# Kernel tuning notes

Hardware: AMD Instinct MI355X
Metric: run time of the kernel (lower is better)

The kernel has to match this reference:

```python
import jax, jax.numpy as jnp
import numpy as np

B, C, T = 128, 295, 2048
D1 = 270
NUM_SUBJECTS = 64

def setup_inputs() -> dict:
    key = jax.random.key(0)
    k_x, k_s, k_w1, k_b1, k_ws = jax.random.split(key, 5)
    X = jax.random.normal(k_x, (B, C, T), dtype=jnp.float32)
    subject_idxs = jax.random.randint(k_s, (B,), 0, NUM_SUBJECTS)
    W1 = jax.random.normal(k_w1, (D1, C), dtype=jnp.float32) * 0.05
    b1 = jax.random.normal(k_b1, (D1,), dtype=jnp.float32) * 0.05
    Ws = jax.random.normal(k_ws, (NUM_SUBJECTS, D1, D1), dtype=jnp.float32) * 0.05
    return {"X": X, "subject_idxs": subject_idxs, "W1": W1, "b1": b1, "Ws": Ws}

def reference(X, subject_idxs, W1, b1, Ws):
    # Shared 1x1 conv: pointwise channel mix C -> D1 with bias.  [B, D1, T]
    y = jnp.einsum('dc,bct->bdt', W1, X) + b1[None, :, None]
    # Top-1 expert dispatch: gather each sample's subject matrix. [B, D1, D1]
    W_sel = Ws[subject_idxs]
    # Per-sample 1x1 conv (batched GEMM), no bias.            [B, D1, T]
    out = jnp.einsum('bed,bdt->bet', W_sel, y)
    return out
```

## Files before the change

kernel.cpp:

```cpp
#include <hip/hip_runtime.h>
#include <hip/hip_bf16.h>

#define NSUBJ 64
#define CIN   295
#define DD    270
#define TT    2048
#define BB    128

#define WF_PER_S  92160
#define WF_PER_KS 9216
#define W1T_PER_KS 10240

typedef __attribute__((ext_vector_type(8))) short bf16x8;
typedef __attribute__((ext_vector_type(4))) float f32x4;
typedef unsigned short u16;

__device__ __forceinline__ u16 f2bf(float f) {
    return __bfloat16_as_ushort(__float2bfloat16(f));
}

__device__ __forceinline__ void glds16(const void* g, void* lds_base) {
    __builtin_amdgcn_global_load_lds(
        (const __attribute__((address_space(1))) unsigned int*)g,
        (__attribute__((address_space(3))) unsigned int*)lds_base, 16, 0, 0);
}

#define WAITV(N) asm volatile("s_waitcnt vmcnt(" #N ")" ::: "memory")
#define BAR()    __builtin_amdgcn_s_barrier()
#define SB()     __builtin_amdgcn_sched_barrier(0)

__global__ __launch_bounds__(256) void k_prep_w1(const float* __restrict__ W1,
                                                 const float* __restrict__ b1,
                                                 u16* __restrict__ W1t)
{
    const int idx = blockIdx.x * 256 + threadIdx.x;
    const int ks = idx / W1T_PER_KS;
    const int r  = idx - ks * W1T_PER_KS;
    const int kq = r / 2560;
    const int c  = (r - kq * 2560) >> 3;
    const int k8 = r & 7;
    const int d  = ks * 32 + kq * 8 + k8;
    float v = 0.f;
    if (d < DD) {
        if (c < CIN) v = W1[d * CIN + c];
        else if (c == CIN) v = b1[d];
    }
    W1t[idx] = f2bf(v);
}

__global__ __launch_bounds__(256, 1) void k_fuse_w(const float* __restrict__ Ws,
                                                   const u16* __restrict__ W1t,
                                                   u16* __restrict__ Wf)
{
    __shared__ u16 Aw[3072];
    __shared__ u16 Bw[10240];
    const int tid = threadIdx.x, lane = tid & 63, wid = tid >> 6;
    const int wm = wid >> 1, wn = wid & 1;
    const int mt = blockIdx.x, s = blockIdx.y;
    const int e0 = mt * 96;
    const float* Wsb = Ws + (size_t)s * DD * DD;

    f32x4 acc[3][10];
#pragma unroll
    for (int i = 0; i < 3; ++i)
#pragma unroll
        for (int j = 0; j < 10; ++j) acc[i][j] = (f32x4){0.f, 0.f, 0.f, 0.f};

    for (int ks = 0; ks < 9; ++ks) {
        const int k0 = ks * 32;
#pragma unroll
        for (int ci = 0; ci < 3; ++ci) {
            const int id = tid + ci * 256;
            const int m = id >> 3, q = id & 7;
            const int e = e0 + m, d = k0 + q * 4;
            float2 v01 = {0.f, 0.f}, v23 = {0.f, 0.f};
            if (e < DD) {
                if (d < DD)     v01 = *(const float2*)(Wsb + (size_t)e * DD + d);
                if (d + 2 < DD) v23 = *(const float2*)(Wsb + (size_t)e * DD + d + 2);
            }
            ushort4 h;
            h.x = f2bf(v01.x); h.y = f2bf(v01.y); h.z = f2bf(v23.x); h.w = f2bf(v23.y);
            *(ushort4*)(&Aw[(q >> 1) * 768 + m * 8 + (q & 1) * 4]) = h;
        }
#pragma unroll
        for (int k5 = 0; k5 < 5; ++k5) {
            const int seg = wid * 5 + k5;
            glds16(W1t + (size_t)ks * W1T_PER_KS + seg * 512 + lane * 8, &Bw[seg * 512]);
        }
        __syncthreads();
        bf16x8 af[3];
#pragma unroll
        for (int i = 0; i < 3; ++i)
            af[i] = *(const bf16x8*)(&Aw[(lane >> 4) * 768 + (wm * 48 + i * 16 + (lane & 15)) * 8]);
#pragma unroll
        for (int j = 0; j < 10; ++j) {
            const bf16x8 bfj = *(const bf16x8*)(&Bw[(lane >> 4) * 2560 + (wn * 160 + j * 16 + (lane & 15)) * 8]);
#pragma unroll
            for (int i = 0; i < 3; ++i)
                acc[i][j] = __builtin_amdgcn_mfma_f32_16x16x32_bf16(af[i], bfj, acc[i][j], 0, 0, 0);
        }
        __syncthreads();
    }
    const int rb = (lane >> 4) * 4, cc = lane & 15;
#pragma unroll
    for (int i = 0; i < 3; ++i) {
#pragma unroll
        for (int r = 0; r < 4; ++r) {
            const int e = e0 + wm * 48 + i * 16 + rb + r;
#pragma unroll
            for (int j = 0; j < 10; ++j) {
                const int c = wn * 160 + j * 16 + cc;
                Wf[(size_t)s * WF_PER_S + (c >> 5) * WF_PER_KS + ((c >> 3) & 3) * 2304
                   + e * 8 + (c & 7)] = f2bf(acc[i][j][r]);
            }
        }
    }
}

__global__ __launch_bounds__(256, 2) void k_main(const float* __restrict__ X,
                                                 const int* __restrict__ subj,
                                                 const u16* __restrict__ Wf,
                                                 float* __restrict__ out)
{
    __shared__ u16   Am[3][9216];
    __shared__ float Xm[3][2048];
    const int tid = threadIdx.x, lane = tid & 63, wid = tid >> 6;
    const int wm = wid >> 1, wn = wid & 1;
    const int hw = blockIdx.x;
    const int w  = (hw & 7) * 512 + (hw >> 3);
    const int b  = w >> 5, nt = w & 31;
    const int t0 = nt * 64;
    const int s = subj[b];
    const float* Xb = X + (size_t)b * CIN * TT;
    const u16* WfA = Wf + (size_t)s * WF_PER_S;
    const int g = lane >> 4;

    f32x4 acc[9][2];
#pragma unroll
    for (int i = 0; i < 9; ++i)
#pragma unroll
        for (int j = 0; j < 2; ++j) acc[i][j] = (f32x4){0.f, 0.f, 0.f, 0.f};

#define STAGEA(KS, BUF)                                                     \
    {                                                                       \
        _Pragma("unroll")                                                   \
        for (int k5 = 0; k5 < 5; ++k5) {                                    \
            const int seg = wid + 4 * k5;                                   \
            if (seg < 18)                                                   \
                glds16(WfA + (size_t)(KS) * WF_PER_KS + seg * 512 + lane * 8,\
                       &Am[BUF][seg * 512]);                                \
        }                                                                   \
    }
#define STAGEX(KS, BUF)                                                     \
    {                                                                       \
        _Pragma("unroll")                                                   \
        for (int k2 = 0; k2 < 2; ++k2) {                                    \
            const int seg = wid * 2 + k2;                                   \
            const int cr0 = (KS) * 32 + seg * 4 + g;                        \
            const int cr  = (cr0 < CIN) ? cr0 : (CIN - 1);                  \
            const int sc  = (lane & 15) ^ (((seg >> 1) & 3) << 2);          \
            glds16(Xb + (size_t)cr * TT + t0 + sc * 4,                      \
                   &Xm[BUF][seg * 256]);                                    \
        }                                                                   \
    }
#define WAITSTEP()  { if (wid < 2) WAITV(7); else WAITV(6); }

#define COMPUTE(BUF, LAST)                                                  \
    {                                                                       \
        const float* Xc = &Xm[BUF][0];                                      \
        bf16x8 bfr[2];                                                      \
        _Pragma("unroll")                                                   \
        for (int j = 0; j < 2; ++j) {                                       \
            const int tsw = (wn * 32 + j * 16 + (lane & 15)) ^ (g << 4);    \
            bf16x8 bb;                                                      \
            _Pragma("unroll")                                               \
            for (int q = 0; q < 8; ++q) {                                   \
                float v = Xc[(g * 8 + q) * 64 + tsw];                       \
                if (LAST) {                                                 \
                    if (q == 7)      v = (g == 0) ? 1.0f : 0.0f;            \
                    else if (g > 0)  v = 0.0f;                              \
                }                                                           \
                bb[q] = (short)f2bf(v);                                     \
            }                                                               \
            bfr[j] = bb;                                                    \
        }                                                                   \
        _Pragma("unroll")                                                   \
        for (int i = 0; i < 9; ++i) {                                       \
            const bf16x8 af = *(const bf16x8*)(&Am[BUF][g * 2304 + (wm * 144 + i * 16 + (lane & 15)) * 8]); \
            acc[i][0] = __builtin_amdgcn_mfma_f32_16x16x32_bf16(af, bfr[0], acc[i][0], 0, 0, 0); \
            acc[i][1] = __builtin_amdgcn_mfma_f32_16x16x32_bf16(af, bfr[1], acc[i][1], 0, 0, 0); \
        }                                                                   \
    }

    STAGEA(0, 0); STAGEX(0, 0); SB();
    STAGEA(1, 1); STAGEX(1, 1); SB();
    WAITSTEP();
    BAR();

#define STEP(K)                                                             \
    {                                                                       \
        STAGEA((K) + 2, ((K) + 2) % 3); STAGEX((K) + 2, ((K) + 2) % 3); SB();\
        COMPUTE((K) % 3, 0);                                                \
        WAITSTEP();                                                         \
        BAR();                                                              \
    }
    STEP(0) STEP(1) STEP(2) STEP(3) STEP(4) STEP(5) STEP(6) STEP(7)
    COMPUTE(2, 0);
    WAITV(0);
    BAR();
    COMPUTE(0, 1);

    const int rb = g * 4, cc = lane & 15;
#pragma unroll
    for (int i = 0; i < 9; ++i) {
#pragma unroll
        for (int r = 0; r < 4; ++r) {
            const int e = wm * 144 + i * 16 + rb + r;
            if (e < DD) {
#pragma unroll
                for (int j = 0; j < 2; ++j) {
                    const int t = t0 + wn * 32 + j * 16 + cc;
                    out[((size_t)b * DD + e) * TT + t] = acc[i][j][r];
                }
            }
        }
    }
#undef STAGEA
#undef STAGEX
#undef WAITSTEP
#undef COMPUTE
#undef STEP
}

extern "C" void kernel_launch(void* const* d_in, const int* in_sizes, int n_in,
                              void* d_out, int out_size, void* d_ws, size_t ws_size,
                              hipStream_t stream) {
    const float* X    = (const float*)d_in[0];
    const int*   subj = (const int*)d_in[1];
    const float* W1   = (const float*)d_in[2];
    const float* b1   = (const float*)d_in[3];
    const float* Ws   = (const float*)d_in[4];
    float* out = (float*)d_out;

    u16* Wf  = (u16*)d_ws;
    u16* W1t = (u16*)((char*)d_ws + (size_t)NSUBJ * WF_PER_S * 2);

    k_prep_w1<<<dim3(360), 256, 0, stream>>>(W1, b1, W1t);
    k_fuse_w<<<dim3(3, NSUBJ), 256, 0, stream>>>(Ws, W1t, Wf);
    k_main<<<dim3(TT / 64 * BB), 256, 0, stream>>>(X, subj, Wf, out);
}
```

Measured before the change: 184.8 us.

## Make main kernel persistent over eight tiles with cross-tile prefetch

The main GEMM kernel now launches 512 blocks, and each block loops over eight consecutive output tiles instead of handling one tile per block. The first two K-stages of the next tile are prefetched while the last stages and epilogue of the current tile run, and the triple-buffer pointers are rotated between tiles. This targets block launch, prologue and pipeline drain costs. The trade-offs are fewer resident blocks relative to CU count, which may hurt load balance, and more complex wait/barrier logic.

Measured after the change: 179.8 us. 2.7% less time.

```diff
diff --git a/kernel.cpp b/kernel.cpp
--- a/kernel.cpp
+++ b/kernel.cpp
@@ -122,18 +122,20 @@
                                                  const u16* __restrict__ Wf,
                                                  float* __restrict__ out)
 {
-    __shared__ u16   Am[3][9216];
-    __shared__ float Xm[3][2048];
+    __shared__ u16   AmBuf[3][9216];
+    __shared__ float XmBuf[3][2048];
     const int tid = threadIdx.x, lane = tid & 63, wid = tid >> 6;
     const int wm = wid >> 1, wn = wid & 1;
+    const int g = lane >> 4, l15 = lane & 15;
     const int hw = blockIdx.x;
-    const int w  = (hw & 7) * 512 + (hw >> 3);
-    const int b  = w >> 5, nt = w & 31;
-    const int t0 = nt * 64;
-    const int s = subj[b];
+    int w = (hw & 7) * 512 + (hw >> 3) * 8;
+    int b = w >> 5;
+    int t0 = (w & 31) * 64;
     const float* Xb = X + (size_t)b * CIN * TT;
-    const u16* WfA = Wf + (size_t)s * WF_PER_S;
-    const int g = lane >> 4;
+    const u16*  WfA = Wf + (size_t)subj[b] * WF_PER_S;
+
+    u16   *amA = &AmBuf[0][0], *amB = &AmBuf[1][0], *amC = &AmBuf[2][0];
+    float *xmA = &XmBuf[0][0], *xmB = &XmBuf[1][0], *xmC = &XmBuf[2][0];
 
     f32x4 acc[9][2];
 #pragma unroll
@@ -141,41 +143,40 @@
 #pragma unroll
         for (int j = 0; j < 2; ++j) acc[i][j] = (f32x4){0.f, 0.f, 0.f, 0.f};
 
-#define STAGEA(KS, BUF)                                                     \
+#define STAGEA_TO(KS, DST, WFP)                                             \
     {                                                                       \
         _Pragma("unroll")                                                   \
         for (int k5 = 0; k5 < 5; ++k5) {                                    \
             const int seg = wid + 4 * k5;                                   \
             if (seg < 18)                                                   \
-                glds16(WfA + (size_t)(KS) * WF_PER_KS + seg * 512 + lane * 8,\
-                       &Am[BUF][seg * 512]);                                \
-        }                                                                   \
-    }
-#define STAGEX(KS, BUF)                                                     \
+                glds16((WFP) + (size_t)(KS) * WF_PER_KS + seg * 512 + lane * 8,\
+                       (DST) + seg * 512);                                  \
+        }                                                                   \
+    }
+#define STAGEX_TO(KS, DST, XP, T0)                                          \
     {                                                                       \
         _Pragma("unroll")                                                   \
         for (int k2 = 0; k2 < 2; ++k2) {                                    \
             const int seg = wid * 2 + k2;                                   \
             const int cr0 = (KS) * 32 + seg * 4 + g;                        \
             const int cr  = (cr0 < CIN) ? cr0 : (CIN - 1);                  \
-            const int sc  = (lane & 15) ^ (((seg >> 1) & 3) << 2);          \
-            glds16(Xb + (size_t)cr * TT + t0 + sc * 4,                      \
-                   &Xm[BUF][seg * 256]);                                    \
+            const int sc  = l15 ^ (((seg >> 1) & 3) << 2);                  \
+            glds16((XP) + (size_t)cr * TT + (T0) + sc * 4,                  \
+                   (DST) + seg * 256);                                      \
         }                                                                   \
     }
 #define WAITSTEP()  { if (wid < 2) WAITV(7); else WAITV(6); }
 
-#define COMPUTE(BUF, LAST)                                                  \
-    {                                                                       \
-        const float* Xc = &Xm[BUF][0];                                      \
+#define COMPUTE_FROM(AM, XM, LAST)                                          \
+    {                                                                       \
         bf16x8 bfr[2];                                                      \
         _Pragma("unroll")                                                   \
         for (int j = 0; j < 2; ++j) {                                       \
-            const int tsw = (wn * 32 + j * 16 + (lane & 15)) ^ (g << 4);    \
+            const int tsw = (wn * 32 + j * 16 + l15) ^ (g << 4);            \
             bf16x8 bb;                                                      \
             _Pragma("unroll")                                               \
             for (int q = 0; q < 8; ++q) {                                   \
-                float v = Xc[(g * 8 + q) * 64 + tsw];                       \
+                float v = (XM)[(g * 8 + q) * 64 + tsw];                     \
                 if (LAST) {                                                 \
                     if (q == 7)      v = (g == 0) ? 1.0f : 0.0f;            \
                     else if (g > 0)  v = 0.0f;                              \
@@ -186,50 +187,84 @@
         }                                                                   \
         _Pragma("unroll")                                                   \
         for (int i = 0; i < 9; ++i) {                                       \
-            const bf16x8 af = *(const bf16x8*)(&Am[BUF][g * 2304 + (wm * 144 + i * 16 + (lane & 15)) * 8]); \
+            const bf16x8 af = *(const bf16x8*)((AM) + g * 2304 + (wm * 144 + i * 16 + l15) * 8); \
             acc[i][0] = __builtin_amdgcn_mfma_f32_16x16x32_bf16(af, bfr[0], acc[i][0], 0, 0, 0); \
             acc[i][1] = __builtin_amdgcn_mfma_f32_16x16x32_bf16(af, bfr[1], acc[i][1], 0, 0, 0); \
         }                                                                   \
     }
-
-    STAGEA(0, 0); STAGEX(0, 0); SB();
-    STAGEA(1, 1); STAGEX(1, 1); SB();
+#define STEPN(K, DAM, DXM, CAM, CXM)                                        \
+    {                                                                       \
+        STAGEA_TO((K) + 2, DAM, WfA); STAGEX_TO((K) + 2, DXM, Xb, t0); SB();\
+        COMPUTE_FROM(CAM, CXM, 0);                                          \
+        WAITSTEP();                                                         \
+        BAR();                                                              \
+    }
+
+    STAGEA_TO(0, amA, WfA); STAGEX_TO(0, xmA, Xb, t0); SB();
+    STAGEA_TO(1, amB, WfA); STAGEX_TO(1, xmB, Xb, t0); SB();
     WAITSTEP();
     BAR();
 
-#define STEP(K)                                                             \
-    {                                                                       \
-        STAGEA((K) + 2, ((K) + 2) % 3); STAGEX((K) + 2, ((K) + 2) % 3); SB();\
-        COMPUTE((K) % 3, 0);                                                \
-        WAITSTEP();                                                         \
-        BAR();                                                              \
-    }
-    STEP(0) STEP(1) STEP(2) STEP(3) STEP(4) STEP(5) STEP(6) STEP(7)
-    COMPUTE(2, 0);
-    WAITV(0);
-    BAR();
-    COMPUTE(0, 1);
-
-    const int rb = g * 4, cc = lane & 15;
-#pragma unroll
-    for (int i = 0; i < 9; ++i) {
-#pragma unroll
-        for (int r = 0; r < 4; ++r) {
-            const int e = wm * 144 + i * 16 + rb + r;
-            if (e < DD) {
-#pragma unroll
-                for (int j = 0; j < 2; ++j) {
-                    const int t = t0 + wn * 32 + j * 16 + cc;
-                    out[((size_t)b * DD + e) * TT + t] = acc[i][j][r];
+#pragma unroll 1
+    for (int it = 0; it < 8; ++it) {
+        const bool more = (it < 7);
+        const int  w2  = more ? (w + 1) : w;
+        const int  b2  = w2 >> 5;
+        const int  t02 = (w2 & 31) * 64;
+        const float* XbN = X + (size_t)b2 * CIN * TT;
+        const u16*  WfAN = Wf + (size_t)subj[b2] * WF_PER_S;
+
+        STEPN(0, amC, xmC, amA, xmA)
+        STEPN(1, amA, xmA, amB, xmB)
+        STEPN(2, amB, xmB, amC, xmC)
+        STEPN(3, amC, xmC, amA, xmA)
+        STEPN(4, amA, xmA, amB, xmB)
+        STEPN(5, amB, xmB, amC, xmC)
+        STEPN(6, amC, xmC, amA, xmA)
+        STEPN(7, amA, xmA, amB, xmB)
+        if (more) { STAGEA_TO(0, amB, WfAN); STAGEX_TO(0, xmB, XbN, t02); SB(); }
+        COMPUTE_FROM(amC, xmC, 0);
+        if (more) { WAITSTEP(); }
+        else      { WAITV(0); }
+        BAR();
+        if (more) { STAGEA_TO(1, amC, WfAN); STAGEX_TO(1, xmC, XbN, t02); SB(); }
+        COMPUTE_FROM(amA, xmA, 1);
+
+        {
+            const int rb = g * 4;
+#pragma unroll
+            for (int i = 0; i < 9; ++i) {
+#pragma unroll
+                for (int r = 0; r < 4; ++r) {
+                    const int e = wm * 144 + i * 16 + rb + r;
+                    if (e < DD) {
+#pragma unroll
+                        for (int j = 0; j < 2; ++j) {
+                            const int t = t0 + wn * 32 + j * 16 + l15;
+                            out[((size_t)b * DD + e) * TT + t] = acc[i][j][r];
+                        }
+                    }
                 }
             }
         }
-    }
-#undef STAGEA
-#undef STAGEX
+#pragma unroll
+        for (int i = 0; i < 9; ++i)
+#pragma unroll
+            for (int j = 0; j < 2; ++j) acc[i][j] = (f32x4){0.f, 0.f, 0.f, 0.f};
+
+        if (more) {
+            WAITV(63);
+            BAR();
+            u16*   ta = amA; amA = amB; amB = amC; amC = ta;
+            float* tx = xmA; xmA = xmB; xmB = xmC; xmC = tx;
+            w = w2; b = b2; t0 = t02; Xb = XbN; WfA = WfAN;
+        }
+    }
+#undef STAGEA_TO
+#undef STAGEX_TO
 #undef WAITSTEP
-#undef COMPUTE
-#undef STEP
+#undef COMPUTE_FROM
+#undef STEPN
 }
 
 extern "C" void kernel_launch(void* const* d_in, const int* in_sizes, int n_in,
@@ -247,5 +282,5 @@
 
     k_prep_w1<<<dim3(360), 256, 0, stream>>>(W1, b1, W1t);
     k_fuse_w<<<dim3(3, NSUBJ), 256, 0, stream>>>(Ws, W1t, Wf);
-    k_main<<<dim3(TT / 64 * BB), 256, 0, stream>>>(X, subj, Wf, out);
-}
+    k_main<<<dim3(512), 256, 0, stream>>>(X, subj, Wf, out);
+}
```

## Load subject weight fragments directly from global into registers instead of LDS

Applied to the files above, without the earlier changes.

The per-subject fused weight operand is no longer staged through a triple-buffered LDS array with global_load_lds. Each wave now reads its own bf16x8 A fragments straight from global memory (L2) at the start of each K-step, and only the X tile stays in LDS. This frees about 55 KB of LDS per block and drops the A-staging instructions and the per-wave split wait counts. The cost is that each fragment load is issued right before the MFMAs that use it, so its latency is exposed. Ordering with the LDS-DMA X prefetch now depends on in-order vmcnt waits the compiler inserts for those loads.

After: 206.3 us. 11.6% more time.

```diff
diff --git a/kernel.cpp b/kernel.cpp
--- a/kernel.cpp
+++ b/kernel.cpp
@@ -122,18 +122,17 @@
                                                  const u16* __restrict__ Wf,
                                                  float* __restrict__ out)
 {
-    __shared__ u16   Am[3][9216];
     __shared__ float Xm[3][2048];
     const int tid = threadIdx.x, lane = tid & 63, wid = tid >> 6;
     const int wm = wid >> 1, wn = wid & 1;
+    const int g = lane >> 4, l15 = lane & 15;
     const int hw = blockIdx.x;
     const int w  = (hw & 7) * 512 + (hw >> 3);
     const int b  = w >> 5, nt = w & 31;
     const int t0 = nt * 64;
     const int s = subj[b];
     const float* Xb = X + (size_t)b * CIN * TT;
-    const u16* WfA = Wf + (size_t)s * WF_PER_S;
-    const int g = lane >> 4;
+    const u16* aB = Wf + (size_t)s * WF_PER_S + g * 2304 + (wm * 144 + l15) * 8;
 
     f32x4 acc[9][2];
 #pragma unroll
@@ -141,37 +140,29 @@
 #pragma unroll
         for (int j = 0; j < 2; ++j) acc[i][j] = (f32x4){0.f, 0.f, 0.f, 0.f};
 
-#define STAGEA(KS, BUF)                                                     \
-    {                                                                       \
-        _Pragma("unroll")                                                   \
-        for (int k5 = 0; k5 < 5; ++k5) {                                    \
-            const int seg = wid + 4 * k5;                                   \
-            if (seg < 18)                                                   \
-                glds16(WfA + (size_t)(KS) * WF_PER_KS + seg * 512 + lane * 8,\
-                       &Am[BUF][seg * 512]);                                \
-        }                                                                   \
-    }
-#define STAGEX(KS, BUF)                                                     \
+#define STAGEX(KS)                                                          \
     {                                                                       \
         _Pragma("unroll")                                                   \
         for (int k2 = 0; k2 < 2; ++k2) {                                    \
             const int seg = wid * 2 + k2;                                   \
             const int cr0 = (KS) * 32 + seg * 4 + g;                        \
             const int cr  = (cr0 < CIN) ? cr0 : (CIN - 1);                  \
-            const int sc  = (lane & 15) ^ (((seg >> 1) & 3) << 2);          \
+            const int sc  = l15 ^ (((seg >> 1) & 3) << 2);                  \
             glds16(Xb + (size_t)cr * TT + t0 + sc * 4,                      \
-                   &Xm[BUF][seg * 256]);                                    \
+                   &Xm[(KS) % 3][seg * 256]);                               \
         }                                                                   \
     }
-#define WAITSTEP()  { if (wid < 2) WAITV(7); else WAITV(6); }
-
-#define COMPUTE(BUF, LAST)                                                  \
+#define COMPUTE(KS, LAST)                                                   \
     {                                                                       \
-        const float* Xc = &Xm[BUF][0];                                      \
+        bf16x8 af[9];                                                       \
+        _Pragma("unroll")                                                   \
+        for (int i = 0; i < 9; ++i)                                         \
+            af[i] = *(const bf16x8*)(aB + (size_t)(KS) * WF_PER_KS + i * 128);\
+        const float* Xc = &Xm[(KS) % 3][0];                                 \
         bf16x8 bfr[2];                                                      \
         _Pragma("unroll")                                                   \
         for (int j = 0; j < 2; ++j) {                                       \
-            const int tsw = (wn * 32 + j * 16 + (lane & 15)) ^ (g << 4);    \
+            const int tsw = (wn * 32 + j * 16 + l15) ^ (g << 4);            \
             bf16x8 bb;                                                      \
             _Pragma("unroll")                                               \
             for (int q = 0; q < 8; ++q) {                                   \
@@ -186,31 +177,27 @@
         }                                                                   \
         _Pragma("unroll")                                                   \
         for (int i = 0; i < 9; ++i) {                                       \
-            const bf16x8 af = *(const bf16x8*)(&Am[BUF][g * 2304 + (wm * 144 + i * 16 + (lane & 15)) * 8]); \
-            acc[i][0] = __builtin_amdgcn_mfma_f32_16x16x32_bf16(af, bfr[0], acc[i][0], 0, 0, 0); \
-            acc[i][1] = __builtin_amdgcn_mfma_f32_16x16x32_bf16(af, bfr[1], acc[i][1], 0, 0, 0); \
+            acc[i][0] = __builtin_amdgcn_mfma_f32_16x16x32_bf16(af[i], bfr[0], acc[i][0], 0, 0, 0); \
+            acc[i][1] = __builtin_amdgcn_mfma_f32_16x16x32_bf16(af[i], bfr[1], acc[i][1], 0, 0, 0); \
         }                                                                   \
     }
 
-    STAGEA(0, 0); STAGEX(0, 0); SB();
-    STAGEA(1, 1); STAGEX(1, 1); SB();
-    WAITSTEP();
+    STAGEX(0); STAGEX(1); SB();
+    WAITV(2);
     BAR();
 
 #define STEP(K)                                                             \
     {                                                                       \
-        STAGEA((K) + 2, ((K) + 2) % 3); STAGEX((K) + 2, ((K) + 2) % 3); SB();\
-        COMPUTE((K) % 3, 0);                                                \
-        WAITSTEP();                                                         \
+        STAGEX((K) + 2); SB();                                              \
+        COMPUTE(K, 0);                                                      \
         BAR();                                                              \
     }
     STEP(0) STEP(1) STEP(2) STEP(3) STEP(4) STEP(5) STEP(6) STEP(7)
-    COMPUTE(2, 0);
-    WAITV(0);
+    COMPUTE(8, 0);
     BAR();
-    COMPUTE(0, 1);
-
-    const int rb = g * 4, cc = lane & 15;
+    COMPUTE(9, 1);
+
+    const int rb = g * 4;
 #pragma unroll
     for (int i = 0; i < 9; ++i) {
 #pragma unroll
@@ -219,15 +206,13 @@
             if (e < DD) {
 #pragma unroll
                 for (int j = 0; j < 2; ++j) {
-                    const int t = t0 + wn * 32 + j * 16 + cc;
+                    const int t = t0 + wn * 32 + j * 16 + l15;
                     out[((size_t)b * DD + e) * TT + t] = acc[i][j][r];
                 }
             }
         }
     }
-#undef STAGEA
 #undef STAGEX
-#undef WAITSTEP
 #undef COMPUTE
 #undef STEP
 }
```
